# Performance work log

Hardware: AMD Instinct MI355X
Metric: run time of the kernel (lower is better)

Reference implementation:

```python
import jax, jax.numpy as jnp
import numpy as np

N_NODES = 100000
N_EDGES = 3200000
IN_DIM = 512
HID_DIM = 16
OUT_DIM = 64


def _gcn_layer(E, X, W, b, n_nodes):
    # Standard GCN layer (CatGNN GCNLayer_MPNN_2):
    # add self-loops, symmetric deg^-1/2 normalization, project, gather-scatter sum.
    src = jnp.concatenate([E[0], jnp.arange(n_nodes, dtype=E.dtype)])
    dst = jnp.concatenate([E[1], jnp.arange(n_nodes, dtype=E.dtype)])
    deg = jax.ops.segment_sum(jnp.ones_like(dst, dtype=X.dtype), dst, num_segments=n_nodes)
    dinv = jnp.where(deg > 0, jax.lax.rsqrt(deg), 0.0)  # deg^-1/2, safe
    h = X @ W  # [N, d_out] project BEFORE aggregation (cheaper gather)
    norm = dinv[src] * dinv[dst]  # [E+N]
    msg = h[src] * norm[:, None]  # gather + scale
    out = jax.ops.segment_sum(msg, dst, num_segments=n_nodes)  # scatter-sum
    return out + b


def setup_inputs() -> dict:
    key = jax.random.key(0)
    k1, k2, k3, k4, k5 = jax.random.split(key, 5)
    V = jnp.arange(N_NODES, dtype=jnp.int64)
    E = jax.random.randint(k1, (2, N_EDGES), 0, N_NODES, dtype=jnp.int64)
    X = jax.random.normal(k2, (N_NODES, IN_DIM), dtype=jnp.float32)
    # Glorot-style init for layer weights
    W1 = jax.random.normal(k3, (IN_DIM, HID_DIM), dtype=jnp.float32) / np.sqrt(IN_DIM)
    b1 = jnp.zeros((HID_DIM,), dtype=jnp.float32)
    W2 = jax.random.normal(k4, (HID_DIM, OUT_DIM), dtype=jnp.float32) / np.sqrt(HID_DIM)
    b2 = jnp.zeros((OUT_DIM,), dtype=jnp.float32)
    return {"V": V, "E": E, "X": X, "W1": W1, "b1": b1, "W2": W2, "b2": b2}


def reference(V, E, X, W1, b1, W2, b2):
    n_nodes = V.shape[0]
    H = jax.nn.relu(_gcn_layer(E, X, W1, b1, n_nodes))
    # dropout is identity in eval mode
    H = _gcn_layer(E, H, W2, b2, n_nodes)
    return H
```

## Files before the change

### kernel.cpp

```cpp
#include <hip/hip_runtime.h>

#define HID 16
#define ODIM 64
#define IDIM 512
#define BKB 8
#define BKS 256
#define PTILE 4096
#define MAXBE 12288

__global__ __launch_bounds__(256) void k_bhist(const int* __restrict__ dst,
                                               int* __restrict__ bcnt, int ne, int nbk) {
    __shared__ int h[512];
    for (int t = threadIdx.x; t < 512; t += 256) h[t] = 0;
    __syncthreads();
    int stride = gridDim.x * blockDim.x;
    for (int e = blockIdx.x * blockDim.x + threadIdx.x; e < ne; e += stride)
        atomicAdd(&h[dst[e] >> BKB], 1);
    __syncthreads();
    for (int t = threadIdx.x; t < nbk; t += 256)
        if (h[t]) atomicAdd(&bcnt[t], h[t]);
}

__global__ __launch_bounds__(512) void k_bscan(const int* __restrict__ bcnt,
                                               int* __restrict__ bbase,
                                               int* __restrict__ bcur, int nbk) {
    __shared__ int s[512];
    int t = threadIdx.x;
    int v = (t < nbk) ? bcnt[t] : 0;
    s[t] = v;
    __syncthreads();
    for (int off = 1; off < 512; off <<= 1) {
        int u = (t >= off) ? s[t - off] : 0;
        __syncthreads();
        s[t] += u;
        __syncthreads();
    }
    if (t < nbk) { int b = s[t] - v; bbase[t] = b; bcur[t] = b; }
}

__global__ __launch_bounds__(512) void k_part(const int* __restrict__ src,
                                              const int* __restrict__ dst,
                                              int* __restrict__ bcur,
                                              unsigned int* __restrict__ ebuf,
                                              int ne, int nbk) {
    __shared__ int h[512], sc[512], base[512], lcur[512];
    __shared__ unsigned int sval[PTILE];
    __shared__ int saddr[PTILE];
    int e0 = blockIdx.x * PTILE;
    int m = ne - e0; if (m > PTILE) m = PTILE;
    if (m <= 0) return;
    int t = threadIdx.x;
    h[t] = 0;
    __syncthreads();
    for (int k = t; k < m; k += 512) atomicAdd(&h[dst[e0 + k] >> BKB], 1);
    __syncthreads();
    int hv = h[t];
    sc[t] = hv;
    __syncthreads();
    for (int off = 1; off < 512; off <<= 1) {
        int u = (t >= off) ? sc[t - off] : 0;
        __syncthreads();
        sc[t] += u;
        __syncthreads();
    }
    base[t] = hv ? atomicAdd(&bcur[t], hv) : 0;
    lcur[t] = 0;
    __syncthreads();
    for (int k = t; k < m; k += 512) {
        int d = dst[e0 + k];
        int b = d >> BKB;
        int r = atomicAdd(&lcur[b], 1);
        int slot = sc[b] - h[b] + r;
        sval[slot] = ((unsigned int)src[e0 + k] << BKB) | (unsigned int)(d & (BKS - 1));
        saddr[slot] = base[b] + r;
    }
    __syncthreads();
    for (int k = t; k < m; k += 512) ebuf[saddr[k]] = sval[k];
}

__global__ __launch_bounds__(512) void k_csr(const int* __restrict__ bbase,
                                             const int* __restrict__ bcnt,
                                             const unsigned int* __restrict__ ebuf,
                                             int* __restrict__ cnt,
                                             int* __restrict__ row_start,
                                             int* __restrict__ csr_src, int n) {
    __shared__ int h[256], sc[256], lc[256];
    __shared__ int stage[MAXBE];
    int bk = blockIdx.x;
    int node0 = bk << BKB;
    int ebase = bbase[bk];
    int ecnt = bcnt[bk];
    int t = threadIdx.x;
    if (t < 256) { h[t] = 0; lc[t] = 0; }
    __syncthreads();
    for (int k = t; k < ecnt; k += 512) atomicAdd(&h[ebuf[ebase + k] & (BKS - 1)], 1);
    __syncthreads();
    int hv = (t < 256) ? h[t] : 0;
    if (t < 256) sc[t] = hv;
    __syncthreads();
    for (int off = 1; off < 256; off <<= 1) {
        int u = (t >= off && t < 256) ? sc[t - off] : 0;
        __syncthreads();
        if (t < 256) sc[t] += u;
        __syncthreads();
    }
    if (t < 256) {
        int node = node0 + t;
        if (node < n) { cnt[node] = hv; row_start[node] = ebase + sc[t] - hv; }
    }
    if (ecnt <= MAXBE) {
        for (int k = t; k < ecnt; k += 512) {
            unsigned int p = ebuf[ebase + k];
            int dl = p & (BKS - 1);
            int r = atomicAdd(&lc[dl], 1);
            stage[sc[dl] - h[dl] + r] = (int)(p >> BKB);
        }
        __syncthreads();
        for (int k = t; k < ecnt; k += 512) csr_src[ebase + k] = stage[k];
    } else {
        for (int k = t; k < ecnt; k += 512) {
            unsigned int p = ebuf[ebase + k];
            int dl = p & (BKS - 1);
            int r = atomicAdd(&lc[dl], 1);
            csr_src[ebase + sc[dl] - h[dl] + r] = (int)(p >> BKB);
        }
    }
}

__device__ __forceinline__ void fmaq(float4& a, float s, float4 w) {
    a.x = fmaf(s, w.x, a.x);
    a.y = fmaf(s, w.y, a.y);
    a.z = fmaf(s, w.z, a.z);
    a.w = fmaf(s, w.w, a.w);
}

__global__ __launch_bounds__(256) void k_proj1(const float* __restrict__ X,
                                               const float* __restrict__ W1,
                                               const int* __restrict__ cnt,
                                               float* __restrict__ hs1, int n) {
    int i = blockIdx.x * 256 + threadIdx.x;
    if (i >= n) return;

    const float4* __restrict__ xr = (const float4*)(X + (size_t)i * IDIM);
    const float4* __restrict__ W4 = (const float4*)W1;
    float4 a0 = make_float4(0.f, 0.f, 0.f, 0.f), a1 = a0, a2 = a0, a3 = a0;

#pragma unroll 4
    for (int k4 = 0; k4 < IDIM / 4; ++k4) {
        float4 x = xr[k4];
        const float4* w = W4 + k4 * 16;
        fmaq(a0, x.x, w[0]);  fmaq(a1, x.x, w[1]);  fmaq(a2, x.x, w[2]);  fmaq(a3, x.x, w[3]);
        fmaq(a0, x.y, w[4]);  fmaq(a1, x.y, w[5]);  fmaq(a2, x.y, w[6]);  fmaq(a3, x.y, w[7]);
        fmaq(a0, x.z, w[8]);  fmaq(a1, x.z, w[9]);  fmaq(a2, x.z, w[10]); fmaq(a3, x.z, w[11]);
        fmaq(a0, x.w, w[12]); fmaq(a1, x.w, w[13]); fmaq(a2, x.w, w[14]); fmaq(a3, x.w, w[15]);
    }

    float di = rsqrtf((float)(cnt[i] + 1));
    a0.x *= di; a0.y *= di; a0.z *= di; a0.w *= di;
    a1.x *= di; a1.y *= di; a1.z *= di; a1.w *= di;
    a2.x *= di; a2.y *= di; a2.z *= di; a2.w *= di;
    a3.x *= di; a3.y *= di; a3.z *= di; a3.w *= di;
    float4* h4 = (float4*)(hs1 + (size_t)i * HID);
    h4[0] = a0; h4[1] = a1; h4[2] = a2; h4[3] = a3;
}

__device__ __forceinline__ void acc4(float4& a, float4 v) {
    a.x += v.x; a.y += v.y; a.z += v.z; a.w += v.w;
}

__device__ __forceinline__ float4 gacc(int rs, int c, int q,
                                       const int* __restrict__ csr_src,
                                       const float4* __restrict__ h4,
                                       float4 acc) {
    float4 acc2 = make_float4(0.f, 0.f, 0.f, 0.f);
    int k = 0;
    int head = (-rs) & 3;
    if (head > c) head = c;
    for (; k < head; ++k)
        acc4(acc, h4[(size_t)csr_src[rs + k] * 4 + q]);
    for (; k + 7 < c; k += 8) {
        int4 s0 = *(const int4*)(csr_src + rs + k);
        int4 s1 = *(const int4*)(csr_src + rs + k + 4);
        float4 v0 = h4[(size_t)s0.x * 4 + q];
        float4 v1 = h4[(size_t)s0.y * 4 + q];
        float4 v2 = h4[(size_t)s0.z * 4 + q];
        float4 v3 = h4[(size_t)s0.w * 4 + q];
        float4 w0 = h4[(size_t)s1.x * 4 + q];
        float4 w1 = h4[(size_t)s1.y * 4 + q];
        float4 w2 = h4[(size_t)s1.z * 4 + q];
        float4 w3 = h4[(size_t)s1.w * 4 + q];
        acc4(acc, v0);  acc4(acc2, w0);
        acc4(acc, v1);  acc4(acc2, w1);
        acc4(acc, v2);  acc4(acc2, w2);
        acc4(acc, v3);  acc4(acc2, w3);
    }
    for (; k + 3 < c; k += 4) {
        int4 s = *(const int4*)(csr_src + rs + k);
        acc4(acc, h4[(size_t)s.x * 4 + q]);
        acc4(acc2, h4[(size_t)s.y * 4 + q]);
        acc4(acc, h4[(size_t)s.z * 4 + q]);
        acc4(acc2, h4[(size_t)s.w * 4 + q]);
    }
    for (; k < c; ++k)
        acc4(acc, h4[(size_t)csr_src[rs + k] * 4 + q]);
    acc4(acc, acc2);
    return acc;
}

__global__ __launch_bounds__(256) void k_gather_mid(const int* __restrict__ row_start,
                                                    const int* __restrict__ cnt,
                                                    const int* __restrict__ csr_src,
                                                    const float* __restrict__ hs,
                                                    const float* __restrict__ b1,
                                                    float* __restrict__ outbuf, int n) {
    int tid = blockIdx.x * blockDim.x + threadIdx.x;
    int i = tid >> 2;
    int q = tid & 3;
    if (i >= n) return;
    const float4* h4 = (const float4*)hs;
    int rs = row_start[i];
    int c = cnt[i];
    float4 acc = gacc(rs, c, q, csr_src, h4, h4[(size_t)i * 4 + q]);
    float di = rsqrtf((float)(c + 1));
    float4 b = ((const float4*)b1)[q];
    float4 r;
    r.x = fmaxf(fmaf(di, acc.x, b.x), 0.f) * di;
    r.y = fmaxf(fmaf(di, acc.y, b.y), 0.f) * di;
    r.z = fmaxf(fmaf(di, acc.z, b.z), 0.f) * di;
    r.w = fmaxf(fmaf(di, acc.w, b.w), 0.f) * di;
    ((float4*)outbuf)[(size_t)i * 4 + q] = r;
}

__global__ __launch_bounds__(256) void k_gather(const int* __restrict__ row_start,
                                                const int* __restrict__ cnt,
                                                const int* __restrict__ csr_src,
                                                const float* __restrict__ hs,
                                                float* __restrict__ agg, int n) {
    int tid = blockIdx.x * blockDim.x + threadIdx.x;
    int i = tid >> 2;
    int q = tid & 3;
    if (i >= n) return;
    const float4* h4 = (const float4*)hs;
    int rs = row_start[i];
    int c = cnt[i];
    float4 acc = gacc(rs, c, q, csr_src, h4, h4[(size_t)i * 4 + q]);
    ((float4*)agg)[(size_t)i * 4 + q] = acc;
}

__global__ __launch_bounds__(256) void k_out(const int* __restrict__ cnt,
                                             const float* __restrict__ agg2,
                                             const float* __restrict__ W2,
                                             const float* __restrict__ b2,
                                             float* __restrict__ out, int n) {
    __shared__ float Ws[HID * ODIM];
    __shared__ float bs[ODIM];
    int t = threadIdx.x;
    for (int u = t; u < HID * ODIM; u += 256) Ws[u] = W2[u];
    if (t < ODIM) bs[t] = b2[t];
    __syncthreads();

    int j = t & 63;
    int slot = t >> 6;
    int i0 = blockIdx.x * 16 + slot * 4;

    float wc[HID];
#pragma unroll
    for (int k = 0; k < HID; ++k) wc[k] = Ws[k * ODIM + j];
    float bj = bs[j];

    const float4* g4 = (const float4*)agg2;
#pragma unroll
    for (int u = 0; u < 4; ++u) {
        int i = i0 + u;
        if (i < n) {
            float4 g0 = g4[(size_t)i * 4 + 0];
            float4 g1 = g4[(size_t)i * 4 + 1];
            float4 g2 = g4[(size_t)i * 4 + 2];
            float4 g3 = g4[(size_t)i * 4 + 3];
            float acc = g0.x * wc[0]  + g0.y * wc[1]  + g0.z * wc[2]  + g0.w * wc[3]
                      + g1.x * wc[4]  + g1.y * wc[5]  + g1.z * wc[6]  + g1.w * wc[7]
                      + g2.x * wc[8]  + g2.y * wc[9]  + g2.z * wc[10] + g2.w * wc[11]
                      + g3.x * wc[12] + g3.y * wc[13] + g3.z * wc[14] + g3.w * wc[15];
            float di = rsqrtf((float)(cnt[i] + 1));
            out[(size_t)i * ODIM + j] = fmaf(di, acc, bj);
        }
    }
}

extern "C" void kernel_launch(void* const* d_in, const int* in_sizes, int n_in,
                              void* d_out, int out_size, void* d_ws, size_t ws_size,
                              hipStream_t stream) {
    const int* E = (const int*)d_in[1];
    const float* X = (const float*)d_in[2];
    const float* W1 = (const float*)d_in[3];
    const float* b1 = (const float*)d_in[4];
    const float* W2 = (const float*)d_in[5];
    const float* b2 = (const float*)d_in[6];
    float* out = (float*)d_out;

    const int n = in_sizes[0];
    const int ne = in_sizes[1] / 2;
    const int* src = E;
    const int* dst = E + ne;
    const int nbk = (n + BKS - 1) >> BKB;

    char* ws = (char*)d_ws;
    int* bcnt = (int*)ws;
    int* bbase = (int*)(ws + (8u << 10));
    int* bcur = (int*)(ws + (16u << 10));
    int* cnt = (int*)(ws + (1u << 20));
    int* row_start = (int*)(ws + (2u << 20));
    unsigned int* ebuf = (unsigned int*)(ws + (3u << 20));
    float* B1 = (float*)(ws + (3u << 20));
    float* B2 = (float*)(ws + (10u << 20));
    int* csr_src = (int*)(ws + (17u << 20));

    hipMemsetAsync(bcnt, 0, nbk * sizeof(int), stream);
    k_bhist<<<1024, 256, 0, stream>>>(dst, bcnt, ne, nbk);
    k_bscan<<<1, 512, 0, stream>>>(bcnt, bbase, bcur, nbk);
    k_part<<<(ne + PTILE - 1) / PTILE, 512, 0, stream>>>(src, dst, bcur, ebuf, ne, nbk);
    k_csr<<<nbk, 512, 0, stream>>>(bbase, bcnt, ebuf, cnt, row_start, csr_src, n);

    k_proj1<<<(n + 255) / 256, 256, 0, stream>>>(X, W1, cnt, B1, n);
    k_gather_mid<<<(n * 4 + 255) / 256, 256, 0, stream>>>(row_start, cnt, csr_src, B1, b1, B2, n);
    k_gather<<<(n * 4 + 255) / 256, 256, 0, stream>>>(row_start, cnt, csr_src, B2, B1, n);
    k_out<<<(n + 15) / 16, 256, 0, stream>>>(cnt, B1, W2, b2, out, n);
}
```

Measured before the change: 509.4 us.

## Use wave-shuffle scans, padded global counters, larger partition tiles, register-held dst

Replaces the shared-memory Hillis-Steele scans in bscan, part and csr with a wave-level shuffle scan that needs only two block barriers. Global bucket counters are padded to separate cache lines to reduce atomic contention, the partition tile is doubled with dst values cached in registers to avoid reloading them, and the histogram grid is reshaped. The csr kernel drops its LDS staging buffer and scatters directly to global memory, which raises occupancy but gives up coalesced writes.

```diff
diff --git a/kernel.cpp b/kernel.cpp
--- a/kernel.cpp
+++ b/kernel.cpp
@@ -5,77 +5,101 @@
 #define IDIM 512
 #define BKB 8
 #define BKS 256
-#define PTILE 4096
-#define MAXBE 12288
-
-__global__ __launch_bounds__(256) void k_bhist(const int* __restrict__ dst,
+#define PTILE 8192
+#define PITER 16
+#define PAD 16
+
+__device__ __forceinline__ int wave_scan_block(int v, int t, int* wsum) {
+    int lane = t & 63, w = t >> 6;
+    int x = v;
+#pragma unroll
+    for (int off = 1; off < 64; off <<= 1) {
+        int y = __shfl_up(x, off, 64);
+        if (lane >= off) x += y;
+    }
+    if (lane == 63) wsum[w] = x;
+    __syncthreads();
+    if (w == 0) {
+        int s = (lane < 8) ? wsum[lane] : 0;
+#pragma unroll
+        for (int off = 1; off < 8; off <<= 1) {
+            int y = __shfl_up(s, off, 64);
+            if (lane >= off) s += y;
+        }
+        if (lane < 8) wsum[lane] = s;
+    }
+    __syncthreads();
+    return x + (w ? wsum[w - 1] : 0);
+}
+
+__global__ __launch_bounds__(512) void k_bhist(const int* __restrict__ dst,
                                                int* __restrict__ bcnt, int ne, int nbk) {
     __shared__ int h[512];
-    for (int t = threadIdx.x; t < 512; t += 256) h[t] = 0;
-    __syncthreads();
-    int stride = gridDim.x * blockDim.x;
-    for (int e = blockIdx.x * blockDim.x + threadIdx.x; e < ne; e += stride)
+    int t = threadIdx.x;
+    h[t] = 0;
+    __syncthreads();
+    int stride = gridDim.x * 512;
+    for (int e = blockIdx.x * 512 + t; e < ne; e += stride)
         atomicAdd(&h[dst[e] >> BKB], 1);
     __syncthreads();
-    for (int t = threadIdx.x; t < nbk; t += 256)
-        if (h[t]) atomicAdd(&bcnt[t], h[t]);
+    if (t < nbk && h[t]) atomicAdd(&bcnt[t * PAD], h[t]);
 }
 
 __global__ __launch_bounds__(512) void k_bscan(const int* __restrict__ bcnt,
                                                int* __restrict__ bbase,
                                                int* __restrict__ bcur, int nbk) {
-    __shared__ int s[512];
-    int t = threadIdx.x;
-    int v = (t < nbk) ? bcnt[t] : 0;
-    s[t] = v;
-    __syncthreads();
-    for (int off = 1; off < 512; off <<= 1) {
-        int u = (t >= off) ? s[t - off] : 0;
-        __syncthreads();
-        s[t] += u;
-        __syncthreads();
-    }
-    if (t < nbk) { int b = s[t] - v; bbase[t] = b; bcur[t] = b; }
+    __shared__ int wsum[8];
+    int t = threadIdx.x;
+    int v = (t < nbk) ? bcnt[t * PAD] : 0;
+    int inc = wave_scan_block(v, t, wsum);
+    if (t < nbk) { int b = inc - v; bbase[t] = b; bcur[t * PAD] = b; }
 }
 
 __global__ __launch_bounds__(512) void k_part(const int* __restrict__ src,
                                               const int* __restrict__ dst,
                                               int* __restrict__ bcur,
-                                              unsigned int* __restrict__ ebuf,
-                                              int ne, int nbk) {
-    __shared__ int h[512], sc[512], base[512], lcur[512];
+                                              unsigned int* __restrict__ ebuf, int ne) {
+    __shared__ int h[512], sc[512], base[512], lcur[512], wsum[8];
     __shared__ unsigned int sval[PTILE];
     __shared__ int saddr[PTILE];
     int e0 = blockIdx.x * PTILE;
     int m = ne - e0; if (m > PTILE) m = PTILE;
-    if (m <= 0) return;
     int t = threadIdx.x;
     h[t] = 0;
     __syncthreads();
-    for (int k = t; k < m; k += 512) atomicAdd(&h[dst[e0 + k] >> BKB], 1);
+    int dv[PITER];
+#pragma unroll
+    for (int it = 0; it < PITER; ++it) {
+        int k = t + it * 512;
+        int d = 0;
+        if (k < m) { d = dst[e0 + k]; atomicAdd(&h[d >> BKB], 1); }
+        dv[it] = d;
+    }
     __syncthreads();
     int hv = h[t];
-    sc[t] = hv;
-    __syncthreads();
-    for (int off = 1; off < 512; off <<= 1) {
-        int u = (t >= off) ? sc[t - off] : 0;
-        __syncthreads();
-        sc[t] += u;
-        __syncthreads();
-    }
-    base[t] = hv ? atomicAdd(&bcur[t], hv) : 0;
+    int inc = wave_scan_block(hv, t, wsum);
+    sc[t] = inc;
+    base[t] = hv ? atomicAdd(&bcur[t * PAD], hv) : 0;
     lcur[t] = 0;
     __syncthreads();
-    for (int k = t; k < m; k += 512) {
-        int d = dst[e0 + k];
-        int b = d >> BKB;
-        int r = atomicAdd(&lcur[b], 1);
-        int slot = sc[b] - h[b] + r;
-        sval[slot] = ((unsigned int)src[e0 + k] << BKB) | (unsigned int)(d & (BKS - 1));
-        saddr[slot] = base[b] + r;
-    }
-    __syncthreads();
-    for (int k = t; k < m; k += 512) ebuf[saddr[k]] = sval[k];
+#pragma unroll
+    for (int it = 0; it < PITER; ++it) {
+        int k = t + it * 512;
+        if (k < m) {
+            int d = dv[it];
+            int b = d >> BKB;
+            int r = atomicAdd(&lcur[b], 1);
+            int slot = sc[b] - h[b] + r;
+            sval[slot] = ((unsigned int)src[e0 + k] << BKB) | (unsigned int)(d & (BKS - 1));
+            saddr[slot] = base[b] + r;
+        }
+    }
+    __syncthreads();
+#pragma unroll
+    for (int it = 0; it < PITER; ++it) {
+        int k = t + it * 512;
+        if (k < m) ebuf[saddr[k]] = sval[k];
+    }
 }
 
 __global__ __launch_bounds__(512) void k_csr(const int* __restrict__ bbase,
@@ -84,46 +108,29 @@
                                              int* __restrict__ cnt,
                                              int* __restrict__ row_start,
                                              int* __restrict__ csr_src, int n) {
-    __shared__ int h[256], sc[256], lc[256];
-    __shared__ int stage[MAXBE];
+    __shared__ int h[256], sc[256], lc[256], wsum[8];
     int bk = blockIdx.x;
     int node0 = bk << BKB;
     int ebase = bbase[bk];
-    int ecnt = bcnt[bk];
+    int ecnt = bcnt[bk * PAD];
     int t = threadIdx.x;
     if (t < 256) { h[t] = 0; lc[t] = 0; }
     __syncthreads();
     for (int k = t; k < ecnt; k += 512) atomicAdd(&h[ebuf[ebase + k] & (BKS - 1)], 1);
     __syncthreads();
     int hv = (t < 256) ? h[t] : 0;
-    if (t < 256) sc[t] = hv;
-    __syncthreads();
-    for (int off = 1; off < 256; off <<= 1) {
-        int u = (t >= off && t < 256) ? sc[t - off] : 0;
-        __syncthreads();
-        if (t < 256) sc[t] += u;
-        __syncthreads();
-    }
+    int inc = wave_scan_block(hv, t, wsum);
     if (t < 256) {
+        sc[t] = inc;
         int node = node0 + t;
-        if (node < n) { cnt[node] = hv; row_start[node] = ebase + sc[t] - hv; }
-    }
-    if (ecnt <= MAXBE) {
-        for (int k = t; k < ecnt; k += 512) {
-            unsigned int p = ebuf[ebase + k];
-            int dl = p & (BKS - 1);
-            int r = atomicAdd(&lc[dl], 1);
-            stage[sc[dl] - h[dl] + r] = (int)(p >> BKB);
-        }
-        __syncthreads();
-        for (int k = t; k < ecnt; k += 512) csr_src[ebase + k] = stage[k];
-    } else {
-        for (int k = t; k < ecnt; k += 512) {
-            unsigned int p = ebuf[ebase + k];
-            int dl = p & (BKS - 1);
-            int r = atomicAdd(&lc[dl], 1);
-            csr_src[ebase + sc[dl] - h[dl] + r] = (int)(p >> BKB);
-        }
+        if (node < n) { cnt[node] = hv; row_start[node] = ebase + inc - hv; }
+    }
+    __syncthreads();
+    for (int k = t; k < ecnt; k += 512) {
+        unsigned int p = ebuf[ebase + k];
+        int dl = p & (BKS - 1);
+        int r = atomicAdd(&lc[dl], 1);
+        csr_src[ebase + sc[dl] - h[dl] + r] = (int)(p >> BKB);
     }
 }
 
@@ -306,8 +313,8 @@
 
     char* ws = (char*)d_ws;
     int* bcnt = (int*)ws;
-    int* bbase = (int*)(ws + (8u << 10));
-    int* bcur = (int*)(ws + (16u << 10));
+    int* bbase = (int*)(ws + (32u << 10));
+    int* bcur = (int*)(ws + (64u << 10));
     int* cnt = (int*)(ws + (1u << 20));
     int* row_start = (int*)(ws + (2u << 20));
     unsigned int* ebuf = (unsigned int*)(ws + (3u << 20));
@@ -315,10 +322,10 @@
     float* B2 = (float*)(ws + (10u << 20));
     int* csr_src = (int*)(ws + (17u << 20));
 
-    hipMemsetAsync(bcnt, 0, nbk * sizeof(int), stream);
-    k_bhist<<<1024, 256, 0, stream>>>(dst, bcnt, ne, nbk);
+    hipMemsetAsync(bcnt, 0, nbk * PAD * sizeof(int), stream);
+    k_bhist<<<256, 512, 0, stream>>>(dst, bcnt, ne, nbk);
     k_bscan<<<1, 512, 0, stream>>>(bcnt, bbase, bcur, nbk);
-    k_part<<<(ne + PTILE - 1) / PTILE, 512, 0, stream>>>(src, dst, bcur, ebuf, ne, nbk);
+    k_part<<<(ne + PTILE - 1) / PTILE, 512, 0, stream>>>(src, dst, bcur, ebuf, ne);
     k_csr<<<nbk, 512, 0, stream>>>(bbase, bcnt, ebuf, cnt, row_start, csr_src, n);
 
     k_proj1<<<(n + 255) / 256, 256, 0, stream>>>(X, W1, cnt, B1, n);
```

Measured after the change: 498.7 us. 2.1% less time.
